# Performance work log

Hardware: AMD Instinct MI355X
Metric: run time of the kernel (lower is better)

The kernel has to match this reference:

```python
import jax, jax.numpy as jnp
import numpy as np
from jax import lax


def build_edges(M, K):
    # star edges keypoint<->root per instrument, plus bidirectional clique over roots
    edges = []
    for m in range(M):
        base = m * K
        root = base + (K - 1)
        for kp in range(K - 1):
            u = base + kp
            edges.append((u, root))
            edges.append((root, u))
    roots = [m * K + (K - 1) for m in range(M)]
    for i in range(len(roots)):
        for j in range(i + 1, len(roots)):
            edges.append((roots[i], roots[j]))
            edges.append((roots[j], roots[i]))
    e = np.asarray(edges, dtype=np.int32).T  # (2, E)
    return jnp.asarray(e[0]), jnp.asarray(e[1])


def lstm(xs, w_ih, w_hh, b_ih, b_hh):
    # xs: (T, BN, in); torch gate order i, f, g, o
    H = w_hh.shape[1]
    BN = xs.shape[1]
    h0 = jnp.zeros((BN, H), xs.dtype)
    c0 = jnp.zeros((BN, H), xs.dtype)

    def step(carry, x):
        h, c = carry
        g = x @ w_ih.T + b_ih + h @ w_hh.T + b_hh
        i, f, gg, o = jnp.split(g, 4, axis=-1)
        c = jax.nn.sigmoid(f) * c + jax.nn.sigmoid(i) * jnp.tanh(gg)
        h = jax.nn.sigmoid(o) * jnp.tanh(c)
        return (h, c), h

    _, hs = lax.scan(step, (h0, c0), xs)
    return hs  # (T, BN, H)


def gat_layer(x, W, a, b, src, dst, N):
    # x: (N, H_in); single-head GAT with LeakyReLU(0.2) scores, ELU output
    h = x @ W                                   # (N, O)
    O = W.shape[1]
    a_src, a_dst = a[:O], a[O:]
    e = jax.nn.leaky_relu(h[src] @ a_src + h[dst] @ a_dst, 0.2)  # (E,)
    emax = jax.ops.segment_max(e, dst, num_segments=N)
    ex = jnp.exp(e - emax[dst])
    denom = jax.ops.segment_sum(ex, dst, num_segments=N)
    alpha = ex / denom[dst]
    out = jax.ops.segment_sum(alpha[:, None] * h[src], dst, num_segments=N) + b
    return jax.nn.elu(out)


def setup_inputs() -> dict:
    key = jax.random.key(0)
    ks = jax.random.split(key, 24)
    B, T, M, K = 64, 128, 8, 5
    E, H = 16, 32
    s = 0.1
    d = {
        'feat': jax.random.uniform(ks[0], (B, T, M, K, 3), jnp.float32),
        'phi_w1': jax.random.normal(ks[1], (3, E)) * s,
        'phi_b1': jax.random.normal(ks[2], (E,)) * s,
        'phi_w2': jax.random.normal(ks[3], (E, E)) * s,
        'phi_b2': jax.random.normal(ks[4], (E,)) * s,
        'spa_wih': jax.random.normal(ks[5], (4 * H, E)) * s,
        'spa_whh': jax.random.normal(ks[6], (4 * H, H)) * s,
        'spa_bih': jax.random.normal(ks[7], (4 * H,)) * s,
        'spa_bhh': jax.random.normal(ks[8], (4 * H,)) * s,
        'bn_gamma': jnp.ones((H,)),
        'bn_beta': jnp.zeros((H,)),
        'gat1_w': jax.random.normal(ks[9], (H, H)) * s,
        'gat1_a': jax.random.normal(ks[10], (2 * H,)) * s,
        'gat1_b': jnp.zeros((H,)),
        'gat2_w': jax.random.normal(ks[11], (H, H)) * s,
        'gat2_a': jax.random.normal(ks[12], (2 * H,)) * s,
        'gat2_b': jnp.zeros((H,)),
        'temp_wih': jax.random.normal(ks[13], (4 * H, H)) * s,
        'temp_whh': jax.random.normal(ks[14], (4 * H, H)) * s,
        'temp_bih': jax.random.normal(ks[15], (4 * H,)) * s,
        'temp_bhh': jax.random.normal(ks[16], (4 * H,)) * s,
    }
    return d


def reference(feat, phi_w1, phi_b1, phi_w2, phi_b2,
              spa_wih, spa_whh, spa_bih, spa_bhh,
              bn_gamma, bn_beta,
              gat1_w, gat1_a, gat1_b, gat2_w, gat2_a, gat2_b,
              temp_wih, temp_whh, temp_bih, temp_bhh):
    B, T, M, K, _ = feat.shape
    # --- add_virtual_root ---
    xy = feat[..., :2]
    vis = feat[..., 2] > 0.5
    w = vis[..., None].astype(feat.dtype)
    denom = jnp.clip(w.sum(axis=3, keepdims=True), 1.0, None)
    root_xy = (xy * w).sum(axis=3, keepdims=True) / denom
    root_vis = jnp.any(vis, axis=3, keepdims=True).astype(feat.dtype)[..., None]
    featR = jnp.concatenate([feat, jnp.concatenate([root_xy, root_vis], -1)], axis=3)
    KR = K + 1
    N = M * KR
    # --- phi MLP ---
    v = jax.nn.relu(featR @ phi_w1 + phi_b1) @ phi_w2 + phi_b2  # (B,T,M,KR,E)
    v = v.reshape(B, T, N, -1)
    # --- spatial LSTM over T, batch B*N ---
    xs = v.transpose(1, 0, 2, 3).reshape(T, B * N, -1)
    H = spa_whh.shape[1]
    r = lstm(xs, spa_wih, spa_whh, spa_bih, spa_bhh).reshape(T, B, N, H).transpose(1, 0, 2, 3)
    # --- per-timestep BatchNorm (training-mode batch stats over B*N) ---
    def bn_t(x_t):  # (B,N,H)
        xf = x_t.reshape(-1, H)
        mu = xf.mean(0)
        var = ((xf - mu) ** 2).mean(0)
        return (x_t - mu) / jnp.sqrt(var + 1e-5) * bn_gamma + bn_beta
    x_bn = jax.vmap(bn_t, in_axes=1, out_axes=1)(r)  # (B,T,N,H)
    # --- two GAT layers per (b,t) graph ---
    src, dst = build_edges(M, KR)
    xflat = x_bn.reshape(B * T, N, H)
    g1 = jax.vmap(lambda z: gat_layer(z, gat1_w, gat1_a, gat1_b, src, dst, N))(xflat)
    g2 = jax.vmap(lambda z: gat_layer(z, gat2_w, gat2_a, gat2_b, src, dst, N))(g1)
    rhat = g2.reshape(B, T, N, H)
    # --- temporal LSTM ---
    temp_in = rhat.transpose(1, 0, 2, 3).reshape(T, B * N, H)
    l = lstm(temp_in, temp_wih, temp_whh, temp_bih, temp_bhh).reshape(T, B, N, H).transpose(1, 0, 2, 3)
    h = jnp.concatenate([r, l], axis=-1)  # (B,T,N,2H)
    return (r, h)
```

## Files before the change

kernel.cpp:

```cpp
#include <hip/hip_runtime.h>

constexpr int B = 64, T = 128, M = 8, KLEAF = 5, KR = 6, N = 48, E = 16, H = 32;
constexpr int BNR = B * N;
constexpr int NG  = B * T;
constexpr int BNP = 16;
constexpr long long R_SIZE = (long long)B * T * N * H;

#define DEVI __device__ __forceinline__

DEVI float frcp(float x) { return __builtin_amdgcn_rcpf(x); }
DEVI float sigm(float x) { return frcp(1.f + __expf(-x)); }
DEVI float tanh_(float x) {
  float a = __expf(2.f * fabsf(x));
  float r = 1.f - 2.f * frcp(a + 1.f);
  return x >= 0.f ? r : -r;
}

__global__ __launch_bounds__(256) void k_phi(
    const float* __restrict__ feat, const float* __restrict__ w1,
    const float* __restrict__ b1, const float* __restrict__ w2,
    const float* __restrict__ b2, float* __restrict__ v_ws)
{
  int gid = blockIdx.x * 256 + threadIdx.x;
  if (gid >= B * T * N) return;
  int nn = gid % N;
  int bt = gid / N;
  int m = nn / KR, k = nn % KR;
  int t = bt % T, b = bt / T;
  const float* fp = feat + ((size_t)bt * M + m) * (KLEAF * 3);
  float x0, x1, x2;
  if (k < KLEAF) {
    x0 = fp[k * 3 + 0]; x1 = fp[k * 3 + 1]; x2 = fp[k * 3 + 2];
  } else {
    float sx = 0.f, sy = 0.f, sw = 0.f, av = 0.f;
#pragma unroll
    for (int kp = 0; kp < KLEAF; kp++) {
      float fx = fp[kp * 3], fy = fp[kp * 3 + 1], fv = fp[kp * 3 + 2];
      float w = fv > 0.5f ? 1.f : 0.f;
      sx += fx * w; sy += fy * w; sw += w; av = fmaxf(av, w);
    }
    float dn = fmaxf(sw, 1.f);
    x0 = sx / dn; x1 = sy / dn; x2 = av;
  }
  float hd[E];
#pragma unroll
  for (int e = 0; e < E; e++) {
    float v = b1[e] + x0 * w1[0 * E + e] + x1 * w1[1 * E + e] + x2 * w1[2 * E + e];
    hd[e] = v > 0.f ? v : 0.f;
  }
  float* vo = v_ws + ((size_t)t * BNR + (size_t)b * N + nn) * E;
#pragma unroll
  for (int e2 = 0; e2 < E; e2++) {
    float acc = b2[e2];
#pragma unroll
    for (int e = 0; e < E; e++) acc += hd[e] * w2[e * E + e2];
    vo[e2] = acc;
  }
}

#define LSTM_STEP(PF, XCUR, XNXT)                                             \
  {                                                                           \
    if (PF) {                                                                 \
      _Pragma("unroll")                                                       \
      for (int q = 0; q < X4; q++) XNXT[q] = xptr[q];                         \
      xptr += XSTRIDE;                                                        \
    }                                                                         \
    float aA0 = bsA, aA1 = 0.f, aA2 = 0.f, aA3 = 0.f;                         \
    float aB0 = bsB, aB1 = 0.f, aB2 = 0.f, aB3 = 0.f;                         \
    _Pragma("unroll")                                                         \
    for (int q = 0; q < X4; q++) {                                            \
      float4 xv = XCUR[q];                                                    \
      aA0 += WxA[4 * q + 0] * xv.x; aA1 += WxA[4 * q + 1] * xv.y;             \
      aA2 += WxA[4 * q + 2] * xv.z; aA3 += WxA[4 * q + 3] * xv.w;             \
      aB0 += WxB[4 * q + 0] * xv.x; aB1 += WxB[4 * q + 1] * xv.y;             \
      aB2 += WxB[4 * q + 2] * xv.z; aB3 += WxB[4 * q + 3] * xv.w;             \
    }                                                                         \
    _Pragma("unroll")                                                         \
    for (int q = 0; q < 8; q++) {                                             \
      float4 hv = ((const float4*)hbuf)[q];                                   \
      aA0 += WhA[4 * q + 0] * hv.x; aA1 += WhA[4 * q + 1] * hv.y;             \
      aA2 += WhA[4 * q + 2] * hv.z; aA3 += WhA[4 * q + 3] * hv.w;             \
      aB0 += WhB[4 * q + 0] * hv.x; aB1 += WhB[4 * q + 1] * hv.y;             \
      aB2 += WhB[4 * q + 2] * hv.z; aB3 += WhB[4 * q + 3] * hv.w;             \
    }                                                                         \
    float aA = (aA0 + aA1) + (aA2 + aA3);                                     \
    float aB = (aB0 + aB1) + (aB2 + aB3);                                     \
    float sA = sigm(aA);                        \
    float vB = hi ? sigm(aB) : tanh_(aB);       \
    float send = hi ? sA : sA * vB;             \
    float recv = __shfl_xor(send, 32);                                        \
    float sF = hi ? sA : recv;                                                \
    float p2 = hi ? recv : send;                                              \
    c = sF * c + p2;                                                          \
    float tc = tanh_(c);                                                      \
    if (hi) {                                                                 \
      float hnew = vB * tc;                                                   \
      hbuf[j] = hnew;                                                         \
      if (MODE == 0) { *pr = hnew; *ph = hnew; }                              \
      else { *ph = hnew; }                                                    \
    }                                                                         \
    pr += N * H; ph += N * 2 * H;                                             \
  }

template <int EE, int MODE>
__global__ __launch_bounds__(256) void k_lstm(
    const float* __restrict__ x, const float* __restrict__ wih,
    const float* __restrict__ whh, const float* __restrict__ bih,
    const float* __restrict__ bhh, float* __restrict__ dout)
{
  constexpr int X4 = EE / 4;
  int lane = threadIdx.x & 63, wid = threadIdx.x >> 6;
  int j = lane & 31, hi = lane >> 5;
  int row = blockIdx.x * 4 + wid;
  int b = row / N, n = row % N;
  int gA = hi * 32 + j, gB = 64 + hi * 32 + j;

  float WxA[EE], WxB[EE], WhA[32], WhB[32];
#pragma unroll
  for (int e = 0; e < EE; e++) { WxA[e] = wih[gA * EE + e]; WxB[e] = wih[gB * EE + e]; }
#pragma unroll
  for (int k = 0; k < 32; k++) { WhA[k] = whh[gA * 32 + k]; WhB[k] = whh[gB * 32 + k]; }
  float bsA = bih[gA] + bhh[gA], bsB = bih[gB] + bhh[gB];

  __shared__ __align__(16) float hbufA[4][32];
  float* hbuf = hbufA[wid];
  if (hi == 0) hbuf[j] = 0.f;

  float c = 0.f;
  constexpr size_t XSTRIDE = (size_t)BNR * EE / 4;
  const float4* xptr = (const float4*)(x + (size_t)row * EE);

  float* pr = dout + ((size_t)b * T * N + n) * H + j;
  float* ph = dout + R_SIZE + ((size_t)b * T * N + n) * 2 * H + (MODE == 1 ? H : 0) + j;

  float4 XC[X4], XN[X4];
#pragma unroll
  for (int q = 0; q < X4; q++) XC[q] = xptr[q];
  xptr += XSTRIDE;

  for (int t = 0; t < T - 2; t += 2) {
    LSTM_STEP(true, XC, XN);
    LSTM_STEP(true, XN, XC);
  }
  LSTM_STEP(true, XC, XN);
  LSTM_STEP(false, XN, XC);
}

__global__ __launch_bounds__(256) void k_bn1(
    const float* __restrict__ r, float* __restrict__ part)
{
  int t = blockIdx.x, p = blockIdx.y;
  int c = threadIdx.x & 31, rg = threadIdx.x >> 5;
  constexpr int RPP = BNR / BNP;
  float s = 0.f, s2 = 0.f;
  for (int row = p * RPP + rg; row < (p + 1) * RPP; row += 8) {
    int b = row / N, n = row % N;
    float x = r[((size_t)b * T + t) * N * H + (size_t)n * H + c];
    s += x; s2 += x * x;
  }
  __shared__ float sm[2][8][32];
  sm[0][rg][c] = s; sm[1][rg][c] = s2;
  __syncthreads();
  if (rg == 0) {
    float ss = 0.f, ss2 = 0.f;
#pragma unroll
    for (int i = 0; i < 8; i++) { ss += sm[0][i][c]; ss2 += sm[1][i][c]; }
    part[((size_t)t * BNP + p) * 64 + c] = ss;
    part[((size_t)t * BNP + p) * 64 + 32 + c] = ss2;
  }
}

__global__ void k_bn2(
    const float* __restrict__ part, const float* __restrict__ gamma,
    const float* __restrict__ beta, float* __restrict__ sctab)
{
  int t = blockIdx.x, c = threadIdx.x;
  float ss = 0.f, ss2 = 0.f;
#pragma unroll
  for (int p = 0; p < BNP; p++) {
    ss  += part[((size_t)t * BNP + p) * 64 + c];
    ss2 += part[((size_t)t * BNP + p) * 64 + 32 + c];
  }
  float mu = ss * (1.f / BNR);
  float var = ss2 * (1.f / BNR) - mu * mu;
  float rstd = rsqrtf(var + 1e-5f);
  float sc = gamma[c] * rstd;
  sctab[t * 64 + c] = sc;
  sctab[t * 64 + 32 + c] = beta[c] - mu * sc;
}

__global__ __launch_bounds__(256) void k_gat(
    const float* __restrict__ r, const float* __restrict__ sctab,
    const float* __restrict__ w1, const float* __restrict__ a1, const float* __restrict__ bg1,
    const float* __restrict__ w2, const float* __restrict__ a2, const float* __restrict__ bg2,
    float* __restrict__ gat_ws)
{
  int g = blockIdx.x;
  int b = g >> 7, t = g & 127;
  int tid = threadIdx.x;
  __shared__ float X[N][H];
  __shared__ float Hm[N][H + 1];
  __shared__ float Wl[H * H];
  __shared__ float ssrc[N], sdst[N];
  __shared__ float alph[M][12];
  for (int i = tid; i < N * H; i += 256) {
    int cc = i & 31;
    ((float*)X)[i] = r[(size_t)g * N * H + i] * sctab[t * 64 + cc] + sctab[t * 64 + 32 + cc];
  }
  const float* Ws[2] = {w1, w2};
  const float* As[2] = {a1, a2};
  const float* Bs[2] = {bg1, bg2};
  int oc = tid & 31, n0 = tid >> 5;
  for (int layer = 0; layer < 2; layer++) {
    const float* av = As[layer];
    const float* bias = Bs[layer];
    for (int i = tid; i < H * H; i += 256) Wl[i] = Ws[layer][i];
    __syncthreads();
#pragma unroll
    for (int rep = 0; rep < 6; rep++) {
      int n = n0 + rep * 8;
      float acc = 0.f;
#pragma unroll
      for (int kk = 0; kk < H; kk++) acc += X[n][kk] * Wl[kk * H + oc];
      Hm[n][oc] = acc;
    }
    __syncthreads();
    if (tid < N) {
      float as = 0.f, ad = 0.f;
#pragma unroll
      for (int kk = 0; kk < H; kk++) {
        float x = Hm[tid][kk];
        as += x * av[kk]; ad += x * av[H + kk];
      }
      ssrc[tid] = as; sdst[tid] = ad;
    }
    __syncthreads();
    if (tid < M) {
      float ev[12];
      float sd = sdst[tid * KR + KR - 1];
#pragma unroll
      for (int kp = 0; kp < KLEAF; kp++) ev[kp] = ssrc[tid * KR + kp] + sd;
#pragma unroll
      for (int j = 0; j < 7; j++) {
        int mm = j < tid ? j : j + 1;
        ev[KLEAF + j] = ssrc[mm * KR + KR - 1] + sd;
      }
      float mx = -1e30f;
#pragma unroll
      for (int i = 0; i < 12; i++) {
        float e = ev[i]; e = e > 0.f ? e : 0.2f * e;
        ev[i] = e; mx = fmaxf(mx, e);
      }
      float s = 0.f;
#pragma unroll
      for (int i = 0; i < 12; i++) { float e = __expf(ev[i] - mx); ev[i] = e; s += e; }
      float inv = frcp(s);
#pragma unroll
      for (int i = 0; i < 12; i++) alph[tid][i] = ev[i] * inv;
    }
    __syncthreads();
    float hv[6];
#pragma unroll
    for (int rep = 0; rep < 6; rep++) {
      int n = n0 + rep * 8;
      int m2 = n / KR;
      float acc;
      if (n % KR == KR - 1) {
        acc = 0.f;
#pragma unroll
        for (int kp = 0; kp < KLEAF; kp++) acc += alph[m2][kp] * Hm[m2 * KR + kp][oc];
#pragma unroll
        for (int j = 0; j < 7; j++) {
          int mm = j < m2 ? j : j + 1;
          acc += alph[m2][KLEAF + j] * Hm[mm * KR + KR - 1][oc];
        }
      } else {
        acc = Hm[m2 * KR + KR - 1][oc];
      }
      acc += bias[oc];
      hv[rep] = acc > 0.f ? acc : __expf(acc) - 1.f;
    }
    __syncthreads();
#pragma unroll
    for (int rep = 0; rep < 6; rep++) X[n0 + rep * 8][oc] = hv[rep];
    __syncthreads();
  }
  for (int i = tid; i < N * H; i += 256)
    gat_ws[((size_t)t * BNR + (size_t)b * N) * H + i] = ((float*)X)[i];
}

extern "C" void kernel_launch(void* const* d_in, const int* in_sizes, int n_in,
                              void* d_out, int out_size, void* d_ws, size_t ws_size,
                              hipStream_t stream)
{
  const float* feat     = (const float*)d_in[0];
  const float* phi_w1   = (const float*)d_in[1];
  const float* phi_b1   = (const float*)d_in[2];
  const float* phi_w2   = (const float*)d_in[3];
  const float* phi_b2   = (const float*)d_in[4];
  const float* spa_wih  = (const float*)d_in[5];
  const float* spa_whh  = (const float*)d_in[6];
  const float* spa_bih  = (const float*)d_in[7];
  const float* spa_bhh  = (const float*)d_in[8];
  const float* bn_gamma = (const float*)d_in[9];
  const float* bn_beta  = (const float*)d_in[10];
  const float* gat1_w   = (const float*)d_in[11];
  const float* gat1_a   = (const float*)d_in[12];
  const float* gat1_b   = (const float*)d_in[13];
  const float* gat2_w   = (const float*)d_in[14];
  const float* gat2_a   = (const float*)d_in[15];
  const float* gat2_b   = (const float*)d_in[16];
  const float* temp_wih = (const float*)d_in[17];
  const float* temp_whh = (const float*)d_in[18];
  const float* temp_bih = (const float*)d_in[19];
  const float* temp_bhh = (const float*)d_in[20];
  float* out = (float*)d_out;

  float* v_ws   = (float*)d_ws;
  float* gat_ws = v_ws   + (size_t)T * BNR * E;
  float* bnpart = gat_ws + (size_t)T * BNR * H;
  float* sctab  = bnpart + (size_t)T * BNP * 64;

  k_phi <<<(B * T * N + 255) / 256, 256, 0, stream>>>(feat, phi_w1, phi_b1, phi_w2, phi_b2, v_ws);
  k_lstm<16, 0><<<BNR / 4, 256, 0, stream>>>(v_ws, spa_wih, spa_whh, spa_bih, spa_bhh, out);
  k_bn1 <<<dim3(T, BNP), 256, 0, stream>>>(out, bnpart);
  k_bn2 <<<T, 32, 0, stream>>>(bnpart, bn_gamma, bn_beta, sctab);
  k_gat <<<NG, 256, 0, stream>>>(out, sctab, gat1_w, gat1_a, gat1_b, gat2_w, gat2_a, gat2_b, gat_ws);
  k_lstm<32, 1><<<BNR / 4, 256, 0, stream>>>(gat_ws, temp_wih, temp_whh, temp_bih, temp_bhh, out);
}
```

Baseline: 478.9 us.

## Split LSTM gate rows across two waves per sequence with LDS exchange

Each LSTM sequence row is now handled by two wavefronts, each computing 64 of the 128 gate pre-activations, instead of one wave computing all 128. This halves per-thread weight registers and dot-product work per step, and doubles the grid size. In exchange, every timestep needs a block-wide __syncthreads and an LDS round trip to combine gates, and the input row is staged through LDS with a prefetch. The serial per-step latency may grow from the barrier, while the extra parallelism and lower register pressure may raise occupancy.

```diff
diff --git a/kernel.cpp b/kernel.cpp
--- a/kernel.cpp
+++ b/kernel.cpp
@@ -58,50 +58,6 @@
   }
 }
 
-#define LSTM_STEP(PF, XCUR, XNXT)                                             \
-  {                                                                           \
-    if (PF) {                                                                 \
-      _Pragma("unroll")                                                       \
-      for (int q = 0; q < X4; q++) XNXT[q] = xptr[q];                         \
-      xptr += XSTRIDE;                                                        \
-    }                                                                         \
-    float aA0 = bsA, aA1 = 0.f, aA2 = 0.f, aA3 = 0.f;                         \
-    float aB0 = bsB, aB1 = 0.f, aB2 = 0.f, aB3 = 0.f;                         \
-    _Pragma("unroll")                                                         \
-    for (int q = 0; q < X4; q++) {                                            \
-      float4 xv = XCUR[q];                                                    \
-      aA0 += WxA[4 * q + 0] * xv.x; aA1 += WxA[4 * q + 1] * xv.y;             \
-      aA2 += WxA[4 * q + 2] * xv.z; aA3 += WxA[4 * q + 3] * xv.w;             \
-      aB0 += WxB[4 * q + 0] * xv.x; aB1 += WxB[4 * q + 1] * xv.y;             \
-      aB2 += WxB[4 * q + 2] * xv.z; aB3 += WxB[4 * q + 3] * xv.w;             \
-    }                                                                         \
-    _Pragma("unroll")                                                         \
-    for (int q = 0; q < 8; q++) {                                             \
-      float4 hv = ((const float4*)hbuf)[q];                                   \
-      aA0 += WhA[4 * q + 0] * hv.x; aA1 += WhA[4 * q + 1] * hv.y;             \
-      aA2 += WhA[4 * q + 2] * hv.z; aA3 += WhA[4 * q + 3] * hv.w;             \
-      aB0 += WhB[4 * q + 0] * hv.x; aB1 += WhB[4 * q + 1] * hv.y;             \
-      aB2 += WhB[4 * q + 2] * hv.z; aB3 += WhB[4 * q + 3] * hv.w;             \
-    }                                                                         \
-    float aA = (aA0 + aA1) + (aA2 + aA3);                                     \
-    float aB = (aB0 + aB1) + (aB2 + aB3);                                     \
-    float sA = sigm(aA);                        \
-    float vB = hi ? sigm(aB) : tanh_(aB);       \
-    float send = hi ? sA : sA * vB;             \
-    float recv = __shfl_xor(send, 32);                                        \
-    float sF = hi ? sA : recv;                                                \
-    float p2 = hi ? recv : send;                                              \
-    c = sF * c + p2;                                                          \
-    float tc = tanh_(c);                                                      \
-    if (hi) {                                                                 \
-      float hnew = vB * tc;                                                   \
-      hbuf[j] = hnew;                                                         \
-      if (MODE == 0) { *pr = hnew; *ph = hnew; }                              \
-      else { *ph = hnew; }                                                    \
-    }                                                                         \
-    pr += N * H; ph += N * 2 * H;                                             \
-  }
-
 template <int EE, int MODE>
 __global__ __launch_bounds__(256) void k_lstm(
     const float* __restrict__ x, const float* __restrict__ wih,
@@ -109,41 +65,80 @@
     const float* __restrict__ bhh, float* __restrict__ dout)
 {
   constexpr int X4 = EE / 4;
-  int lane = threadIdx.x & 63, wid = threadIdx.x >> 6;
+  int tid = threadIdx.x;
+  int wave = tid >> 6;
+  int pr_ = wave >> 1;
+  int wsel = wave & 1;
+  int lane = tid & 63;
   int j = lane & 31, hi = lane >> 5;
-  int row = blockIdx.x * 4 + wid;
+  int row = blockIdx.x * 2 + pr_;
   int b = row / N, n = row % N;
-  int gA = hi * 32 + j, gB = 64 + hi * 32 + j;
-
-  float WxA[EE], WxB[EE], WhA[32], WhB[32];
-#pragma unroll
-  for (int e = 0; e < EE; e++) { WxA[e] = wih[gA * EE + e]; WxB[e] = wih[gB * EE + e]; }
-#pragma unroll
-  for (int k = 0; k < 32; k++) { WhA[k] = whh[gA * 32 + k]; WhB[k] = whh[gB * 32 + k]; }
-  float bsA = bih[gA] + bhh[gA], bsB = bih[gB] + bhh[gB];
-
-  __shared__ __align__(16) float hbufA[4][32];
-  float* hbuf = hbufA[wid];
-  if (hi == 0) hbuf[j] = 0.f;
+  int gate = wsel * 64 + hi * 32 + j;
+
+  float Wx[EE], Wh[32];
+#pragma unroll
+  for (int e = 0; e < EE; e++) Wx[e] = wih[gate * EE + e];
+#pragma unroll
+  for (int k = 0; k < 32; k++) Wh[k] = whh[gate * 32 + k];
+  float bs = bih[gate] + bhh[gate];
+
+  __shared__ __align__(16) float hl[4][32];
+  __shared__ __align__(16) float xl[2][2][EE];
+  __shared__ float gx[2][2][2][2][32];
+
+  if (hi == 0) hl[wave][j] = 0.f;
+  const float* xrow = x + (size_t)row * EE;
+  constexpr size_t XST = (size_t)BNR * EE;
+  if (wsel == 0 && lane < X4)
+    ((float4*)xl[pr_][0])[lane] = ((const float4*)xrow)[lane];
+  __syncthreads();
 
   float c = 0.f;
-  constexpr size_t XSTRIDE = (size_t)BNR * EE / 4;
-  const float4* xptr = (const float4*)(x + (size_t)row * EE);
-
-  float* pr = dout + ((size_t)b * T * N + n) * H + j;
-  float* ph = dout + R_SIZE + ((size_t)b * T * N + n) * 2 * H + (MODE == 1 ? H : 0) + j;
-
-  float4 XC[X4], XN[X4];
-#pragma unroll
-  for (int q = 0; q < X4; q++) XC[q] = xptr[q];
-  xptr += XSTRIDE;
-
-  for (int t = 0; t < T - 2; t += 2) {
-    LSTM_STEP(true, XC, XN);
-    LSTM_STEP(true, XN, XC);
-  }
-  LSTM_STEP(true, XC, XN);
-  LSTM_STEP(false, XN, XC);
+  float* prp = dout + ((size_t)b * T * N + n) * H + j;
+  float* php = dout + R_SIZE + ((size_t)b * T * N + n) * 2 * H + (MODE == 1 ? H : 0) + j;
+
+  for (int t = 0; t < T; t++) {
+    int par = t & 1;
+    float4 xnv = {0, 0, 0, 0};
+    int tn = t + 1 < T ? t + 1 : t;
+    if (wsel == 0 && lane < X4)
+      xnv = ((const float4*)(xrow + (size_t)tn * XST))[lane];
+    float a0 = bs, a1 = 0.f, a2 = 0.f, a3 = 0.f;
+    const float4* xp4 = (const float4*)xl[pr_][par];
+#pragma unroll
+    for (int q = 0; q < X4; q++) {
+      float4 xv = xp4[q];
+      a0 += Wx[4 * q + 0] * xv.x; a1 += Wx[4 * q + 1] * xv.y;
+      a2 += Wx[4 * q + 2] * xv.z; a3 += Wx[4 * q + 3] * xv.w;
+    }
+    const float4* hp4 = (const float4*)hl[wave];
+#pragma unroll
+    for (int q = 0; q < 8; q++) {
+      float4 hv = hp4[q];
+      a0 += Wh[4 * q + 0] * hv.x; a1 += Wh[4 * q + 1] * hv.y;
+      a2 += Wh[4 * q + 2] * hv.z; a3 += Wh[4 * q + 3] * hv.w;
+    }
+    float a = (a0 + a1) + (a2 + a3);
+    float act = (wsel == 0) ? sigm(a) : (hi ? sigm(a) : tanh_(a));
+    gx[pr_][par][wsel][hi][j] = act;
+    if (wsel == 0 && lane < X4)
+      ((float4*)xl[pr_][par ^ 1])[lane] = xnv;
+    __syncthreads();
+    if (hi == 0) {
+      float iv = gx[pr_][par][0][0][j];
+      float fv = gx[pr_][par][0][1][j];
+      float gv = gx[pr_][par][1][0][j];
+      float ov = gx[pr_][par][1][1][j];
+      c = fv * c + iv * gv;
+      float hnew = ov * tanh_(c);
+      hl[wave][j] = hnew;
+      if (wsel == 0) {
+        if (MODE == 0) { *prp = hnew; *php = hnew; }
+        else { *php = hnew; }
+      }
+    }
+    prp += N * H; php += N * 2 * H;
+  }
 }
 
 __global__ __launch_bounds__(256) void k_bn1(
@@ -322,9 +317,9 @@
   float* sctab  = bnpart + (size_t)T * BNP * 64;
 
   k_phi <<<(B * T * N + 255) / 256, 256, 0, stream>>>(feat, phi_w1, phi_b1, phi_w2, phi_b2, v_ws);
-  k_lstm<16, 0><<<BNR / 4, 256, 0, stream>>>(v_ws, spa_wih, spa_whh, spa_bih, spa_bhh, out);
+  k_lstm<16, 0><<<BNR / 2, 256, 0, stream>>>(v_ws, spa_wih, spa_whh, spa_bih, spa_bhh, out);
   k_bn1 <<<dim3(T, BNP), 256, 0, stream>>>(out, bnpart);
   k_bn2 <<<T, 32, 0, stream>>>(bnpart, bn_gamma, bn_beta, sctab);
   k_gat <<<NG, 256, 0, stream>>>(out, sctab, gat1_w, gat1_a, gat1_b, gat2_w, gat2_a, gat2_b, gat_ws);
-  k_lstm<32, 1><<<BNR / 4, 256, 0, stream>>>(gat_ws, temp_wih, temp_whh, temp_bih, temp_bhh, out);
-}
+  k_lstm<32, 1><<<BNR / 2, 256, 0, stream>>>(gat_ws, temp_wih, temp_whh, temp_bih, temp_bhh, out);
+}
```

New measurement: 521.2 us. +8.8%, slower.
